# Kernel tuning notes

Hardware: AMD Instinct MI355X
Metric: run time of the kernel (lower is better)

Reference implementation:

```python
import jax, jax.numpy as jnp
import numpy as np

N_NODE, N_NET, E = 80000, 20000, 150000
H_NODE, H_NET, H_PIN, H_EDGE = 32, 32, 16, 16
OUT_NODE, OUT_NET = 32, 32


def _seg_mean(msgs, dst, num):
    # DGL 'mean' reducer: zero-in-degree destinations get 0 (clamp deg to 1).
    s = jax.ops.segment_sum(msgs, dst, num_segments=num)
    d = jax.ops.segment_sum(jnp.ones((msgs.shape[0],), msgs.dtype), dst, num_segments=num)
    return s / jnp.maximum(d, 1.0)[:, None]


def setup_inputs() -> dict:
    key = jax.random.key(0)
    ks = jax.random.split(key, 14)
    return {
        "node_feat": jax.random.normal(ks[0], (N_NODE, H_NODE), jnp.float32),
        "net_feat": jax.random.normal(ks[1], (N_NET, H_NET), jnp.float32),
        "pin_feat": jax.random.normal(ks[2], (E, H_PIN), jnp.float32),
        "edge_feat": jax.random.normal(ks[3], (E, H_EDGE), jnp.float32),
        "topo_w": jax.random.normal(ks[4], (H_NET * OUT_NODE, H_PIN), jnp.float32) * 0.05,
        "topo_b": jnp.zeros((H_NET * OUT_NODE,), jnp.float32),
        "geom_w": jax.random.normal(ks[5], (H_NODE * OUT_NODE, H_EDGE), jnp.float32) * 0.05,
        "geom_b": jnp.zeros((H_NODE * OUT_NODE,), jnp.float32),
        "gc_w": jax.random.normal(ks[6], (H_NODE, OUT_NET), jnp.float32) * 0.1,
        "gc_b": jnp.zeros((OUT_NET,), jnp.float32),
        "pinned_b": jnp.zeros((OUT_NODE,), jnp.float32),
        "near_b": jnp.zeros((OUT_NODE,), jnp.float32),
        "pins_src": jax.random.randint(ks[7], (E,), 0, N_NODE, dtype=jnp.int32),
        "pins_dst": jax.random.randint(ks[8], (E,), 0, N_NET, dtype=jnp.int32),
        "pinned_src": jax.random.randint(ks[9], (E,), 0, N_NET, dtype=jnp.int32),
        "pinned_dst": jax.random.randint(ks[10], (E,), 0, N_NODE, dtype=jnp.int32),
        "near_src": jax.random.randint(ks[11], (E,), 0, N_NODE, dtype=jnp.int32),
        "near_dst": jax.random.randint(ks[12], (E,), 0, N_NODE, dtype=jnp.int32),
    }


def reference(node_feat, net_feat, pin_feat, edge_feat,
              topo_w, topo_b, geom_w, geom_b, gc_w, gc_b, pinned_b, near_b,
              pins_src, pins_dst, pinned_src, pinned_dst, near_src, near_dst):
    ones_e = jnp.ones((E,), node_feat.dtype)
    # --- 'pins' relation: GraphConv(node -> net), norm='both' ---
    deg_out = jax.ops.segment_sum(ones_e, pins_src, num_segments=N_NODE)
    deg_in = jax.ops.segment_sum(ones_e, pins_dst, num_segments=N_NET)
    norm_src = jax.lax.rsqrt(jnp.maximum(deg_out, 1.0))  # (N_NODE,)
    norm_dst = jax.lax.rsqrt(jnp.maximum(deg_in, 1.0))   # (N_NET,)
    h_src = node_feat * norm_src[:, None]
    agg = jax.ops.segment_sum(h_src[pins_src], pins_dst, num_segments=N_NET)
    net_out = (agg * norm_dst[:, None]) @ gc_w + gc_b  # (N_NET, OUT_NET)

    # --- 'pinned' relation: NNConv(net -> node), edge weight from pin_feat ---
    w_pinned = (pin_feat @ topo_w.T + topo_b).reshape(E, H_NET, OUT_NODE)
    msg_p = jnp.einsum('ei,eio->eo', net_feat[pinned_src], w_pinned)
    pinned_out = _seg_mean(msg_p, pinned_dst, N_NODE) + pinned_b

    # --- 'near' relation: NNConv(node -> node), edge weight from edge_feat ---
    w_near = (edge_feat @ geom_w.T + geom_b).reshape(E, H_NODE, OUT_NODE)
    msg_n = jnp.einsum('ei,eio->eo', node_feat[near_src], w_near)
    near_out = _seg_mean(msg_n, near_dst, N_NODE) + near_b

    # HeteroGraphConv aggregate='max' over relations sharing dst type 'node'
    node_out = jnp.maximum(pinned_out, near_out)
    return node_out, net_out
```

## Files before the change

### kernel.cpp

```cpp
#include <hip/hip_runtime.h>

#define N_NODE 80000
#define N_NET  20000
#define NE     150000
#define WLN    17408

typedef unsigned short u16;
typedef unsigned int u32;
typedef __attribute__((ext_vector_type(8))) short short8v;
typedef __attribute__((ext_vector_type(4))) float f32x4;

static __device__ __forceinline__ u16 f2bf(float f) {
  u32 x = __float_as_uint(f);
  x += 0x7fffu + ((x >> 16) & 1u);
  return (u16)(x >> 16);
}

__global__ __launch_bounds__(256) void wprep_kernel(
    const float* __restrict__ topo_w, const float* __restrict__ topo_b,
    const float* __restrict__ geom_w, const float* __restrict__ geom_b,
    u16* __restrict__ WL0, u16* __restrict__ WL1) {
  int idx = blockIdx.x * 256 + threadIdx.x;
  int rel = idx / WLN;
  int g = idx % WLN;
  int c2h = g >> 9, l = (g >> 3) & 63, j = g & 7;
  int op = l & 15, kg = l >> 4, c = c2h >> 1, h = c2h & 1;
  int i = kg * 8 + j, o = 16 * h + op;
  const float* w = rel ? geom_w : topo_w;
  const float* b = rel ? geom_b : topo_b;
  float v = (c < 16) ? w[(i * 32 + o) * 16 + c] : b[i * 32 + o];
  (rel ? WL1 : WL0)[g] = f2bf(v);
}

__global__ __launch_bounds__(256) void deg_kernel(
    const int* __restrict__ pins_src, const int* __restrict__ pins_dst,
    const int* __restrict__ pinned_dst, const int* __restrict__ near_dst,
    float* __restrict__ deg_out, float* __restrict__ deg_in,
    float* __restrict__ deg_p, float* __restrict__ deg_n) {
  int e = blockIdx.x * 256 + threadIdx.x;
  if (e >= NE) return;
  atomicAdd(deg_out + pins_src[e], 1.0f);
  atomicAdd(deg_in  + pins_dst[e], 1.0f);
  atomicAdd(deg_p   + pinned_dst[e], 1.0f);
  atomicAdd(deg_n   + near_dst[e], 1.0f);
}

__global__ __launch_bounds__(256) void pins_edge_kernel(
    const float* __restrict__ node_feat, const int* __restrict__ src,
    const int* __restrict__ dst, const float* __restrict__ deg_out,
    float* __restrict__ agg) {
  int gid = blockIdx.x * 256 + threadIdx.x;
  int e = gid >> 5;
  if (e >= NE) return;
  int o = gid & 31;
  int s = src[e], d = dst[e];
  float ns = rsqrtf(fmaxf(deg_out[s], 1.0f));
  atomicAdd(agg + (size_t)d * 32 + o, node_feat[(size_t)s * 32 + o] * ns);
}

__global__ __launch_bounds__(512) void nnconv_mfma_kernel(
    const float* __restrict__ feat0, const float* __restrict__ ef0,
    const int* __restrict__ src0, const int* __restrict__ dst0,
    const u16* __restrict__ WL0, float* __restrict__ acc0,
    const float* __restrict__ feat1, const float* __restrict__ ef1,
    const int* __restrict__ src1, const int* __restrict__ dst1,
    const u16* __restrict__ WL1, float* __restrict__ acc1,
    int nb0) {
  __shared__ u16 WS[WLN];
  bool rel = blockIdx.x >= nb0;
  int b = rel ? blockIdx.x - nb0 : blockIdx.x;
  const float* feat = rel ? feat1 : feat0;
  const float* ef   = rel ? ef1 : ef0;
  const int* srcp   = rel ? src1 : src0;
  const int* dstp   = rel ? dst1 : dst0;
  const u16* WLg    = rel ? WL1 : WL0;
  float* acc        = rel ? acc1 : acc0;

  for (int t = threadIdx.x; t < WLN / 8; t += 512)
    ((uint4*)WS)[t] = ((const uint4*)WLg)[t];
  __syncthreads();

  int w = threadIdx.x >> 6, lane = threadIdx.x & 63;
  int er = lane & 15, kg = lane >> 4;

#pragma unroll
  for (int it = 0; it < 2; ++it) {
    int tt = b * 16 + w * 2 + it;
    if (tt >= 9375) continue;
    int e0 = tt * 16;
    int e = e0 + er;
    int s = srcp[e];
    const float* fp = feat + (size_t)s * 32 + kg * 8;
    float4 f0 = *(const float4*)fp;
    float4 f1 = *(const float4*)(fp + 4);
    float4 pq = *(const float4*)(ef + (size_t)e * 16 + kg * 4);
    f32x4 a0 = {0.f, 0.f, 0.f, 0.f}, a1 = {0.f, 0.f, 0.f, 0.f};
#pragma unroll
    for (int c = 0; c < 16; ++c) {
      int srcl = er + 16 * (c >> 2);
      float pc = (c & 3) == 0 ? pq.x : (c & 3) == 1 ? pq.y : (c & 3) == 2 ? pq.z : pq.w;
      float pv = __shfl(pc, srcl, 64);
      u32 d0, d1, d2, d3;
      asm("v_cvt_pk_bf16_f32 %0, %1, %2" : "=v"(d0) : "v"(pv * f0.x), "v"(pv * f0.y));
      asm("v_cvt_pk_bf16_f32 %0, %1, %2" : "=v"(d1) : "v"(pv * f0.z), "v"(pv * f0.w));
      asm("v_cvt_pk_bf16_f32 %0, %1, %2" : "=v"(d2) : "v"(pv * f1.x), "v"(pv * f1.y));
      asm("v_cvt_pk_bf16_f32 %0, %1, %2" : "=v"(d3) : "v"(pv * f1.z), "v"(pv * f1.w));
      short8v af;
      ((u32*)&af)[0] = d0; ((u32*)&af)[1] = d1; ((u32*)&af)[2] = d2; ((u32*)&af)[3] = d3;
      short8v b0 = *(const short8v*)(WS + (c * 2 + 0) * 512 + lane * 8);
      short8v b1 = *(const short8v*)(WS + (c * 2 + 1) * 512 + lane * 8);
      a0 = __builtin_amdgcn_mfma_f32_16x16x32_bf16(af, b0, a0, 0, 0, 0);
      a1 = __builtin_amdgcn_mfma_f32_16x16x32_bf16(af, b1, a1, 0, 0, 0);
    }
    {
      u32 d0, d1, d2, d3;
      asm("v_cvt_pk_bf16_f32 %0, %1, %2" : "=v"(d0) : "v"(f0.x), "v"(f0.y));
      asm("v_cvt_pk_bf16_f32 %0, %1, %2" : "=v"(d1) : "v"(f0.z), "v"(f0.w));
      asm("v_cvt_pk_bf16_f32 %0, %1, %2" : "=v"(d2) : "v"(f1.x), "v"(f1.y));
      asm("v_cvt_pk_bf16_f32 %0, %1, %2" : "=v"(d3) : "v"(f1.z), "v"(f1.w));
      short8v af;
      ((u32*)&af)[0] = d0; ((u32*)&af)[1] = d1; ((u32*)&af)[2] = d2; ((u32*)&af)[3] = d3;
      short8v b0 = *(const short8v*)(WS + 32 * 512 + lane * 8);
      short8v b1 = *(const short8v*)(WS + 33 * 512 + lane * 8);
      a0 = __builtin_amdgcn_mfma_f32_16x16x32_bf16(af, b0, a0, 0, 0, 0);
      a1 = __builtin_amdgcn_mfma_f32_16x16x32_bf16(af, b1, a1, 0, 0, 0);
    }
#pragma unroll
    for (int r = 0; r < 4; ++r) {
      int d = dstp[e0 + kg * 4 + r];
      float* ap = acc + (size_t)d * 32;
      atomicAdd(ap + er, a0[r]);
      atomicAdd(ap + 16 + er, a1[r]);
    }
  }
}

__global__ __launch_bounds__(256) void net_out_kernel(
    const float* __restrict__ agg, const float* __restrict__ deg_in,
    const float* __restrict__ gc_w, const float* __restrict__ gc_b,
    float* __restrict__ out) {
  int gid = blockIdx.x * 256 + threadIdx.x;
  int m = gid >> 5;
  if (m >= N_NET) return;
  int o = gid & 31;
  float nd = rsqrtf(fmaxf(deg_in[m], 1.0f));
  const float* ag = agg + (size_t)m * 32;
  float a = 0.f;
#pragma unroll
  for (int j = 0; j < 32; ++j) a += ag[j] * gc_w[j * 32 + o];
  out[(size_t)N_NODE * 32 + (size_t)m * 32 + o] = a * nd + gc_b[o];
}

__global__ __launch_bounds__(256) void node_out_kernel(
    const float* __restrict__ acc_p, const float* __restrict__ acc_n,
    const float* __restrict__ deg_p, const float* __restrict__ deg_n,
    const float* __restrict__ pinned_b, const float* __restrict__ near_b,
    float* __restrict__ out) {
  int gid = blockIdx.x * 256 + threadIdx.x;
  int v = gid >> 5;
  if (v >= N_NODE) return;
  int o = gid & 31;
  float ap = acc_p[gid] / fmaxf(deg_p[v], 1.0f) + pinned_b[o];
  float an = acc_n[gid] / fmaxf(deg_n[v], 1.0f) + near_b[o];
  out[gid] = fmaxf(ap, an);
}

extern "C" void kernel_launch(void* const* d_in, const int* in_sizes, int n_in,
                              void* d_out, int out_size, void* d_ws, size_t ws_size,
                              hipStream_t stream) {
  const float* node_feat = (const float*)d_in[0];
  const float* net_feat  = (const float*)d_in[1];
  const float* pin_feat  = (const float*)d_in[2];
  const float* edge_feat = (const float*)d_in[3];
  const float* topo_w    = (const float*)d_in[4];
  const float* topo_b    = (const float*)d_in[5];
  const float* geom_w    = (const float*)d_in[6];
  const float* geom_b    = (const float*)d_in[7];
  const float* gc_w      = (const float*)d_in[8];
  const float* gc_b      = (const float*)d_in[9];
  const float* pinned_b  = (const float*)d_in[10];
  const float* near_b    = (const float*)d_in[11];
  const int* pins_src    = (const int*)d_in[12];
  const int* pins_dst    = (const int*)d_in[13];
  const int* pinned_src  = (const int*)d_in[14];
  const int* pinned_dst  = (const int*)d_in[15];
  const int* near_src    = (const int*)d_in[16];
  const int* near_dst    = (const int*)d_in[17];

  char* ws = (char*)d_ws;
  float* acc_p   = (float*)ws;
  float* acc_n   = acc_p + 2560000;
  float* agg     = acc_n + 2560000;
  float* deg_out = agg + 640000;
  float* deg_in  = deg_out + 80000;
  float* deg_p   = deg_in + 20000;
  float* deg_n   = deg_p + 80000;
  size_t zero_bytes = (size_t)6020000 * 4;
  size_t off = (zero_bytes + 255) & ~(size_t)255;
  u16* WL0 = (u16*)(ws + off);  off += (size_t)WLN * 2;
  off = (off + 255) & ~(size_t)255;
  u16* WL1 = (u16*)(ws + off);

  hipMemsetAsync(d_ws, 0, zero_bytes, stream);
  wprep_kernel<<<136, 256, 0, stream>>>(topo_w, topo_b, geom_w, geom_b, WL0, WL1);
  deg_kernel<<<(NE + 255) / 256, 256, 0, stream>>>(pins_src, pins_dst, pinned_dst, near_dst,
                                                   deg_out, deg_in, deg_p, deg_n);
  pins_edge_kernel<<<NE * 32 / 256, 256, 0, stream>>>(node_feat, pins_src, pins_dst, deg_out, agg);
  int nb0 = 586;
  nnconv_mfma_kernel<<<2 * nb0, 512, 0, stream>>>(
      net_feat,  pin_feat,  pinned_src, pinned_dst, WL0, acc_p,
      node_feat, edge_feat, near_src,   near_dst,   WL1, acc_n, nb0);
  net_out_kernel<<<N_NET * 32 / 256, 256, 0, stream>>>(agg, deg_in, gc_w, gc_b, (float*)d_out);
  node_out_kernel<<<N_NODE * 32 / 256, 256, 0, stream>>>(acc_p, acc_n, deg_p, deg_n,
                                                         pinned_b, near_b, (float*)d_out);
}
```

Measured before the change: 211.0 us.

## Replace float atomic scatter with CSR sort-by-destination and gather reductions

Builds CSR structures for each relation (integer histogram, single-block scans, atomic-cursor permutation). The NNConv kernel then processes edges in destination-sorted order and writes per-edge messages to a buffer without atomics. Segment sums for the pins, pinned and near relations become per-destination gather loops, and the weight layout is interleaved so each lane writes a float2. This removes many float atomicAdds and the large memset, but adds three serial passes (one a 3-block scan), a 38MB message buffer, and variable-length per-node loops.

```diff
diff --git a/kernel.cpp b/kernel.cpp
--- a/kernel.cpp
+++ b/kernel.cpp
@@ -4,6 +4,7 @@
 #define N_NET  20000
 #define NE     150000
 #define WLN    17408
+#define NB     586
 
 typedef unsigned short u16;
 typedef unsigned int u32;
@@ -25,46 +26,73 @@
   int g = idx % WLN;
   int c2h = g >> 9, l = (g >> 3) & 63, j = g & 7;
   int op = l & 15, kg = l >> 4, c = c2h >> 1, h = c2h & 1;
-  int i = kg * 8 + j, o = 16 * h + op;
+  int i = kg * 8 + j, o = 2 * op + h;
   const float* w = rel ? geom_w : topo_w;
   const float* b = rel ? geom_b : topo_b;
   float v = (c < 16) ? w[(i * 32 + o) * 16 + c] : b[i * 32 + o];
   (rel ? WL1 : WL0)[g] = f2bf(v);
 }
 
-__global__ __launch_bounds__(256) void deg_kernel(
+__global__ __launch_bounds__(256) void hist_kernel(
     const int* __restrict__ pins_src, const int* __restrict__ pins_dst,
     const int* __restrict__ pinned_dst, const int* __restrict__ near_dst,
-    float* __restrict__ deg_out, float* __restrict__ deg_in,
-    float* __restrict__ deg_p, float* __restrict__ deg_n) {
+    u32* __restrict__ hN, u32* __restrict__ hP, u32* __restrict__ hNr,
+    u32* __restrict__ hS) {
   int e = blockIdx.x * 256 + threadIdx.x;
   if (e >= NE) return;
-  atomicAdd(deg_out + pins_src[e], 1.0f);
-  atomicAdd(deg_in  + pins_dst[e], 1.0f);
-  atomicAdd(deg_p   + pinned_dst[e], 1.0f);
-  atomicAdd(deg_n   + near_dst[e], 1.0f);
-}
-
-__global__ __launch_bounds__(256) void pins_edge_kernel(
-    const float* __restrict__ node_feat, const int* __restrict__ src,
-    const int* __restrict__ dst, const float* __restrict__ deg_out,
-    float* __restrict__ agg) {
-  int gid = blockIdx.x * 256 + threadIdx.x;
-  int e = gid >> 5;
+  atomicAdd(&hN[pins_dst[e]], 1u);
+  atomicAdd(&hP[pinned_dst[e]], 1u);
+  atomicAdd(&hNr[near_dst[e]], 1u);
+  atomicAdd(&hS[pins_src[e]], 1u);
+}
+
+__global__ __launch_bounds__(1024) void scan_kernel(
+    const u32* __restrict__ hN, u32* __restrict__ rpN, u32* __restrict__ curN,
+    const u32* __restrict__ hP, u32* __restrict__ rpP, u32* __restrict__ curP,
+    const u32* __restrict__ hNr, u32* __restrict__ rpNr, u32* __restrict__ curNr) {
+  const u32* h; u32 *rp, *cur; int n;
+  if (blockIdx.x == 0)      { h = hN;  rp = rpN;  cur = curN;  n = N_NET; }
+  else if (blockIdx.x == 1) { h = hP;  rp = rpP;  cur = curP;  n = N_NODE; }
+  else                      { h = hNr; rp = rpNr; cur = curNr; n = N_NODE; }
+  int t = threadIdx.x;
+  int chunk = (n + 1023) / 1024;
+  int lo = t * chunk, hi = min(lo + chunk, n);
+  u32 s = 0;
+  for (int i = lo; i < hi; ++i) s += h[i];
+  __shared__ u32 ps[1024];
+  ps[t] = s;
+  __syncthreads();
+  for (int d = 1; d < 1024; d <<= 1) {
+    u32 v = (t >= d) ? ps[t - d] : 0u;
+    __syncthreads();
+    ps[t] += v;
+    __syncthreads();
+  }
+  u32 r = (t == 0) ? 0u : ps[t - 1];
+  for (int i = lo; i < hi; ++i) { rp[i] = r; cur[i] = r; r += h[i]; }
+  if (t == 1023) rp[n] = ps[1023];
+}
+
+__global__ __launch_bounds__(256) void perm_kernel(
+    const int* __restrict__ pins_src, const int* __restrict__ pins_dst,
+    const int* __restrict__ pinned_dst, const int* __restrict__ near_dst,
+    u32* __restrict__ curN, u32* __restrict__ curP, u32* __restrict__ curNr,
+    u32* __restrict__ permS, u32* __restrict__ permP, u32* __restrict__ permN) {
+  int rel = blockIdx.x / NB;
+  int e = (blockIdx.x % NB) * 256 + threadIdx.x;
   if (e >= NE) return;
-  int o = gid & 31;
-  int s = src[e], d = dst[e];
-  float ns = rsqrtf(fmaxf(deg_out[s], 1.0f));
-  atomicAdd(agg + (size_t)d * 32 + o, node_feat[(size_t)s * 32 + o] * ns);
+  if (rel == 0)      { u32 p = atomicAdd(&curN[pins_dst[e]], 1u);  permS[p] = (u32)pins_src[e]; }
+  else if (rel == 1) { u32 p = atomicAdd(&curP[pinned_dst[e]], 1u);  permP[p] = (u32)e; }
+  else               { u32 p = atomicAdd(&curNr[near_dst[e]], 1u); permN[p] = (u32)e; }
 }
 
 __global__ __launch_bounds__(512) void nnconv_mfma_kernel(
     const float* __restrict__ feat0, const float* __restrict__ ef0,
-    const int* __restrict__ src0, const int* __restrict__ dst0,
-    const u16* __restrict__ WL0, float* __restrict__ acc0,
+    const int* __restrict__ src0, const u32* __restrict__ perm0,
+    const u16* __restrict__ WL0, float* __restrict__ msg0,
     const float* __restrict__ feat1, const float* __restrict__ ef1,
-    const int* __restrict__ src1, const int* __restrict__ dst1,
-    const u16* __restrict__ WL1, float* __restrict__ acc1,
+    const int* __restrict__ src1, const u32* __restrict__ perm1,
+    const u16* __restrict__ WL1, float* __restrict__ msg1,
     int nb0) {
   __shared__ u16 WS[WLN];
   bool rel = blockIdx.x >= nb0;
@@ -72,9 +100,9 @@
   const float* feat = rel ? feat1 : feat0;
   const float* ef   = rel ? ef1 : ef0;
   const int* srcp   = rel ? src1 : src0;
-  const int* dstp   = rel ? dst1 : dst0;
+  const u32* perm   = rel ? perm1 : perm0;
   const u16* WLg    = rel ? WL1 : WL0;
-  float* acc        = rel ? acc1 : acc0;
+  float* msg        = rel ? msg1 : msg0;
 
   for (int t = threadIdx.x; t < WLN / 8; t += 512)
     ((uint4*)WS)[t] = ((const uint4*)WLg)[t];
@@ -88,7 +116,7 @@
     int tt = b * 16 + w * 2 + it;
     if (tt >= 9375) continue;
     int e0 = tt * 16;
-    int e = e0 + er;
+    int e = (int)perm[e0 + er];
     int s = srcp[e];
     const float* fp = feat + (size_t)s * 32 + kg * 8;
     float4 f0 = *(const float4*)fp;
@@ -127,23 +155,40 @@
     }
 #pragma unroll
     for (int r = 0; r < 4; ++r) {
-      int d = dstp[e0 + kg * 4 + r];
-      float* ap = acc + (size_t)d * 32;
-      atomicAdd(ap + er, a0[r]);
-      atomicAdd(ap + 16 + er, a1[r]);
+      int pos = e0 + kg * 4 + r;
+      *(float2*)(msg + (size_t)pos * 32 + er * 2) = make_float2(a0[r], a1[r]);
     }
   }
 }
 
+__global__ __launch_bounds__(256) void agg_gather_kernel(
+    const float* __restrict__ node_feat, const u32* __restrict__ permS,
+    const u32* __restrict__ rpN, const u32* __restrict__ hS,
+    float* __restrict__ agg) {
+  int gid = blockIdx.x * 256 + threadIdx.x;
+  int m = gid >> 4;
+  if (m >= N_NET) return;
+  int p = gid & 15;
+  u32 j0 = rpN[m], j1 = rpN[m + 1];
+  float ax = 0.f, ay = 0.f;
+  for (u32 j = j0; j < j1; ++j) {
+    int s = (int)permS[j];
+    float ns = rsqrtf(fmaxf((float)hS[s], 1.0f));
+    float2 nf = *(const float2*)(node_feat + (size_t)s * 32 + p * 2);
+    ax += ns * nf.x; ay += ns * nf.y;
+  }
+  *(float2*)(agg + (size_t)m * 32 + p * 2) = make_float2(ax, ay);
+}
+
 __global__ __launch_bounds__(256) void net_out_kernel(
-    const float* __restrict__ agg, const float* __restrict__ deg_in,
+    const float* __restrict__ agg, const u32* __restrict__ rpN,
     const float* __restrict__ gc_w, const float* __restrict__ gc_b,
     float* __restrict__ out) {
   int gid = blockIdx.x * 256 + threadIdx.x;
   int m = gid >> 5;
   if (m >= N_NET) return;
   int o = gid & 31;
-  float nd = rsqrtf(fmaxf(deg_in[m], 1.0f));
+  float nd = rsqrtf(fmaxf((float)(rpN[m + 1] - rpN[m]), 1.0f));
   const float* ag = agg + (size_t)m * 32;
   float a = 0.f;
 #pragma unroll
@@ -152,17 +197,32 @@
 }
 
 __global__ __launch_bounds__(256) void node_out_kernel(
-    const float* __restrict__ acc_p, const float* __restrict__ acc_n,
-    const float* __restrict__ deg_p, const float* __restrict__ deg_n,
+    const float* __restrict__ msg_p, const float* __restrict__ msg_n,
+    const u32* __restrict__ rpP, const u32* __restrict__ rpNr,
     const float* __restrict__ pinned_b, const float* __restrict__ near_b,
     float* __restrict__ out) {
   int gid = blockIdx.x * 256 + threadIdx.x;
-  int v = gid >> 5;
+  int v = gid >> 4;
   if (v >= N_NODE) return;
-  int o = gid & 31;
-  float ap = acc_p[gid] / fmaxf(deg_p[v], 1.0f) + pinned_b[o];
-  float an = acc_n[gid] / fmaxf(deg_n[v], 1.0f) + near_b[o];
-  out[gid] = fmaxf(ap, an);
+  int p = gid & 15;
+  u32 a0 = rpP[v], a1 = rpP[v + 1];
+  float px = 0.f, py = 0.f;
+  for (u32 j = a0; j < a1; ++j) {
+    float2 mm = *(const float2*)(msg_p + (size_t)j * 32 + p * 2);
+    px += mm.x; py += mm.y;
+  }
+  float idp = 1.0f / fmaxf((float)(a1 - a0), 1.0f);
+  u32 b0 = rpNr[v], b1 = rpNr[v + 1];
+  float nx = 0.f, ny = 0.f;
+  for (u32 j = b0; j < b1; ++j) {
+    float2 mm = *(const float2*)(msg_n + (size_t)j * 32 + p * 2);
+    nx += mm.x; ny += mm.y;
+  }
+  float idn = 1.0f / fmaxf((float)(b1 - b0), 1.0f);
+  float2 r;
+  r.x = fmaxf(px * idp + pinned_b[2 * p],     nx * idn + near_b[2 * p]);
+  r.y = fmaxf(py * idp + pinned_b[2 * p + 1], ny * idn + near_b[2 * p + 1]);
+  *(float2*)(out + (size_t)v * 32 + p * 2) = r;
 }
 
 extern "C" void kernel_launch(void* const* d_in, const int* in_sizes, int n_in,
@@ -188,29 +248,39 @@
   const int* near_dst    = (const int*)d_in[17];
 
   char* ws = (char*)d_ws;
-  float* acc_p   = (float*)ws;
-  float* acc_n   = acc_p + 2560000;
-  float* agg     = acc_n + 2560000;
-  float* deg_out = agg + 640000;
-  float* deg_in  = deg_out + 80000;
-  float* deg_p   = deg_in + 20000;
-  float* deg_n   = deg_p + 80000;
-  size_t zero_bytes = (size_t)6020000 * 4;
-  size_t off = (zero_bytes + 255) & ~(size_t)255;
-  u16* WL0 = (u16*)(ws + off);  off += (size_t)WLN * 2;
-  off = (off + 255) & ~(size_t)255;
-  u16* WL1 = (u16*)(ws + off);
-
-  hipMemsetAsync(d_ws, 0, zero_bytes, stream);
+  float* msg_p = (float*)ws;
+  float* msg_n = msg_p + 4800000;
+  float* agg   = msg_n + 4800000;
+  u32* hN   = (u32*)(agg + 640000);
+  u32* hP   = hN + 20000;
+  u32* hNr  = hP + 80000;
+  u32* hS   = hNr + 80000;
+  u32* rpN  = hS + 80000;
+  u32* rpP  = rpN + 20001;
+  u32* rpNr = rpP + 80001;
+  u32* curN = rpNr + 80001;
+  u32* curP = curN + 20000;
+  u32* curNr= curP + 80000;
+  u32* permS= curNr + 80000;
+  u32* permP= permS + 150000;
+  u32* permN= permP + 150000;
+  size_t wb = (size_t)((char*)(permN + 150000) - ws);
+  wb = (wb + 255) & ~(size_t)255;
+  u16* WL0 = (u16*)(ws + wb);
+  u16* WL1 = WL0 + WLN;
+
+  hipMemsetAsync(hN, 0, (size_t)260000 * 4, stream);
   wprep_kernel<<<136, 256, 0, stream>>>(topo_w, topo_b, geom_w, geom_b, WL0, WL1);
-  deg_kernel<<<(NE + 255) / 256, 256, 0, stream>>>(pins_src, pins_dst, pinned_dst, near_dst,
-                                                   deg_out, deg_in, deg_p, deg_n);
-  pins_edge_kernel<<<NE * 32 / 256, 256, 0, stream>>>(node_feat, pins_src, pins_dst, deg_out, agg);
-  int nb0 = 586;
-  nnconv_mfma_kernel<<<2 * nb0, 512, 0, stream>>>(
-      net_feat,  pin_feat,  pinned_src, pinned_dst, WL0, acc_p,
-      node_feat, edge_feat, near_src,   near_dst,   WL1, acc_n, nb0);
-  net_out_kernel<<<N_NET * 32 / 256, 256, 0, stream>>>(agg, deg_in, gc_w, gc_b, (float*)d_out);
-  node_out_kernel<<<N_NODE * 32 / 256, 256, 0, stream>>>(acc_p, acc_n, deg_p, deg_n,
+  hist_kernel<<<NB, 256, 0, stream>>>(pins_src, pins_dst, pinned_dst, near_dst,
+                                      hN, hP, hNr, hS);
+  scan_kernel<<<3, 1024, 0, stream>>>(hN, rpN, curN, hP, rpP, curP, hNr, rpNr, curNr);
+  perm_kernel<<<3 * NB, 256, 0, stream>>>(pins_src, pins_dst, pinned_dst, near_dst,
+                                          curN, curP, curNr, permS, permP, permN);
+  nnconv_mfma_kernel<<<2 * NB, 512, 0, stream>>>(
+      net_feat,  pin_feat,  pinned_src, permP, WL0, msg_p,
+      node_feat, edge_feat, near_src,   permN, WL1, msg_n, NB);
+  agg_gather_kernel<<<N_NET * 16 / 256, 256, 0, stream>>>(node_feat, permS, rpN, hS, agg);
+  net_out_kernel<<<N_NET * 32 / 256, 256, 0, stream>>>(agg, rpN, gc_w, gc_b, (float*)d_out);
+  node_out_kernel<<<N_NODE * 16 / 256, 256, 0, stream>>>(msg_p, msg_n, rpP, rpNr,
                                                          pinned_b, near_b, (float*)d_out);
 }
```

Result: slower. 386.8 us (+83.3%).
